# Optimization experiments

Measured on AMD Instinct MI355X. Metric: run time of the kernel, lower is better.

Reference implementation:

```python
import jax, jax.numpy as jnp
import numpy as np


def _chamfer(x, y):
    """pytorch3d.loss.chamfer_distance with defaults:
    mean over points in each direction, sum of the two directions, mean over batch.
    x: [B, N, 3], y: [B, M, 3]; squared Euclidean distances.
    """
    d = (jnp.sum(x * x, axis=-1)[:, :, None]
         + jnp.sum(y * y, axis=-1)[:, None, :]
         - 2.0 * jnp.einsum('bnd,bmd->bnm', x, y))
    cham_x = jnp.mean(jnp.min(d, axis=2), axis=1)  # [B] mean over N of NN dist in y
    cham_y = jnp.mean(jnp.min(d, axis=1), axis=1)  # [B] mean over M of NN dist in x
    return jnp.mean(cham_x) + jnp.mean(cham_y)


def setup_inputs() -> dict:
    key = jax.random.key(0)
    k1, k2, k3 = jax.random.split(key, 3)
    B, N_COARSE, N_FINE, N_GT = 8, 1024, 8192, 8192
    coarse = jax.random.normal(k1, (B, N_COARSE, 3), dtype=jnp.float32)
    fine = jax.random.normal(k2, (B, N_FINE, 3), dtype=jnp.float32)
    gt = jax.random.normal(k3, (B, 3, N_GT), dtype=jnp.float32)  # channel-first, transposed in forward
    alpha = jnp.ones((), dtype=jnp.float32)
    return {"coarse": coarse, "fine": fine, "gt": gt, "alpha": alpha}


def reference(coarse, fine, gt, alpha):
    gt_pts = jnp.transpose(gt, (0, 2, 1))  # [B, N_gt, 3]
    loss_fine = _chamfer(fine, gt_pts)
    loss_coarse = _chamfer(coarse, gt_pts)
    loss = loss_coarse + alpha * loss_fine
    return (loss, loss_coarse, loss_fine)
```

## Files before the change

kernel.cpp:

```cpp
#include <hip/hip_runtime.h>
#include <math.h>

#define TPB 256
#define NF 8192
#define NC 1024
#define NG 8192
#define GRID 4608

#define NMIN 204800
#define RED_BLOCKS 200

typedef _Float16 h8 __attribute__((ext_vector_type(8)));
typedef float fx16 __attribute__((ext_vector_type(16)));

__device__ __forceinline__ float min3f(float a, float b, float c) {
    return fminf(fminf(a, b), c);
}

__global__ __launch_bounds__(TPB) void chamfer_mfma(
    const float* __restrict__ coarse, const float* __restrict__ fine,
    const float* __restrict__ gt, unsigned int* __restrict__ wsmin,
    float* __restrict__ ctrl)
{
    __shared__ __align__(16) _Float16 sA[4096];

    const int bid = blockIdx.x;
    const int tid = threadIdx.x;

    if (bid == 0 && tid < 4) ((unsigned int*)ctrl)[tid] = 0u;

    const float* qp; const float* tp;
    int Nq, Nt; bool qcf, tcf; int batch, qblk, t0, tcount, qbase;

    if (bid < 2048) {
        qp = fine; tp = gt; Nq = NF; Nt = NG; qcf = false; tcf = true;
        batch = bid >> 8; qblk = (bid >> 3) & 31; t0 = (bid & 7) * 1024; tcount = 1024;
        qbase = 0 + batch * NF;
    } else if (bid < 4096) {
        const int r = bid - 2048;
        qp = gt; tp = fine; Nq = NG; Nt = NF; qcf = true; tcf = false;
        batch = r >> 8; qblk = (r >> 3) & 31; t0 = (r & 7) * 1024; tcount = 1024;
        qbase = 65536 + batch * NG;
    } else if (bid < 4352) {
        const int r = bid - 4096;
        qp = coarse; tp = gt; Nq = NC; Nt = NG; qcf = false; tcf = true;
        batch = r >> 5; qblk = (r >> 3) & 3; t0 = (r & 7) * 1024; tcount = 1024;
        qbase = 196608 + batch * NC;
    } else {
        const int r = bid - 4352;
        qp = gt; tp = coarse; Nq = NG; Nt = NC; qcf = true; tcf = false;
        batch = r >> 5; qblk = r & 31; t0 = 0; tcount = 1024;
        qbase = 131072 + batch * NG;
    }

    const int lane = tid & 63;
    const int wave = tid >> 6;
    const int qrow = lane & 31;
    const int kg   = lane >> 5;

    const _Float16 n2  = (_Float16)(-2.0f);
    const _Float16 one = (_Float16)(1.0f);
    const _Float16 zro = (_Float16)(0.0f);

    h8 bq[2]; float qs2[2]; float mmin[2];
#pragma unroll
    for (int j = 0; j < 2; j++) {
        const int qi = qblk * 256 + wave * 64 + j * 32 + qrow;
        float x, y, z;
        if (qcf) {
            x = qp[(size_t)(batch * 3 + 0) * Nq + qi];
            y = qp[(size_t)(batch * 3 + 1) * Nq + qi];
            z = qp[(size_t)(batch * 3 + 2) * Nq + qi];
        } else {
            const float* p = qp + ((size_t)batch * Nq + qi) * 3;
            x = p[0]; y = p[1]; z = p[2];
        }
        qs2[j] = x * x + y * y + z * z;
        const _Float16 xh = (_Float16)x, yh = (_Float16)y, zh = (_Float16)z;
        const _Float16 xl = (_Float16)(x - (float)xh);
        const _Float16 yl = (_Float16)(y - (float)yh);
        const _Float16 zl = (_Float16)(z - (float)zh);
        h8 f;
        if (kg == 0) {
            f[0] = n2 * xh; f[1] = n2 * yh; f[2] = n2 * zh;
            f[3] = n2 * xh; f[4] = n2 * yh; f[5] = n2 * zh;
            f[6] = n2 * xl; f[7] = n2 * yl;
        } else {
            f[0] = n2 * zl; f[1] = one; f[2] = one;
            f[3] = zro; f[4] = zro; f[5] = zro; f[6] = zro; f[7] = zro;
        }
        bq[j] = f;
        mmin[j] = INFINITY;
    }

    const fx16 zacc = {0.f,0.f,0.f,0.f,0.f,0.f,0.f,0.f,
                       0.f,0.f,0.f,0.f,0.f,0.f,0.f,0.f};

    for (int base = 0; base < tcount; base += 256) {
        const int tj = t0 + base + tid;
        float x, y, z;
        if (tcf) {
            x = tp[(size_t)(batch * 3 + 0) * Nt + tj];
            y = tp[(size_t)(batch * 3 + 1) * Nt + tj];
            z = tp[(size_t)(batch * 3 + 2) * Nt + tj];
        } else {
            const float* p = tp + ((size_t)batch * Nt + tj) * 3;
            x = p[0]; y = p[1]; z = p[2];
        }
        const float s = x * x + y * y + z * z;
        const _Float16 xh = (_Float16)x, yh = (_Float16)y, zh = (_Float16)z;
        const _Float16 xl = (_Float16)(x - (float)xh);
        const _Float16 yl = (_Float16)(y - (float)yh);
        const _Float16 zl = (_Float16)(z - (float)zh);
        const _Float16 sh = (_Float16)s;
        const _Float16 sl = (_Float16)(s - (float)sh);
        h8 k0, k1;
        k0[0] = xh; k0[1] = yh; k0[2] = zh; k0[3] = xl;
        k0[4] = yl; k0[5] = zl; k0[6] = xh; k0[7] = yh;
        k1[0] = zh; k1[1] = sh; k1[2] = sl; k1[3] = zro;
        k1[4] = zro; k1[5] = zro; k1[6] = zro; k1[7] = zro;

        __syncthreads();
        const int tr = tid & 31, tt = tid >> 5;
        *(h8*)&sA[tt * 512 + tr * 8]       = k0;
        *(h8*)&sA[tt * 512 + 256 + tr * 8] = k1;
        __syncthreads();

#pragma unroll 4
        for (int tile = 0; tile < 8; tile++) {
            const h8 af = *(const h8*)&sA[tile * 512 + lane * 8];
            const fx16 d0 = __builtin_amdgcn_mfma_f32_32x32x16_f16(af, bq[0], zacc, 0, 0, 0);
            const fx16 d1 = __builtin_amdgcn_mfma_f32_32x32x16_f16(af, bq[1], zacc, 0, 0, 0);
            mmin[0] = min3f(min3f(min3f(d0[0], d0[1], d0[2]),
                                  min3f(d0[3], d0[4], d0[5]),
                                  min3f(d0[6], d0[7], d0[8])),
                            min3f(min3f(d0[9], d0[10], d0[11]),
                                  min3f(d0[12], d0[13], d0[14]),
                                  d0[15]),
                            mmin[0]);
            mmin[1] = min3f(min3f(min3f(d1[0], d1[1], d1[2]),
                                  min3f(d1[3], d1[4], d1[5]),
                                  min3f(d1[6], d1[7], d1[8])),
                            min3f(min3f(d1[9], d1[10], d1[11]),
                                  min3f(d1[12], d1[13], d1[14]),
                                  d1[15]),
                            mmin[1]);
        }
    }

#pragma unroll
    for (int j = 0; j < 2; j++)
        mmin[j] = fminf(mmin[j], __shfl_xor(mmin[j], 32));

    const int qi = qblk * 256 + wave * 64 + kg * 32 + qrow;
    const float d = mmin[kg] + qs2[kg];
    atomicMin(&wsmin[qbase + qi], __float_as_uint(d));
}

__global__ __launch_bounds__(256) void reduce_final_kernel(
    const uint4* __restrict__ wsmin4,
    float* __restrict__ ctrl,
    const float* __restrict__ alpha,
    float* __restrict__ out)
{
    __shared__ float red0[4], red1[4];
    const int tid = threadIdx.x;
    const int i = blockIdx.x * 256 + tid;

    const uint4 v = wsmin4[i];
    const float sum4 = __uint_as_float(v.x) + __uint_as_float(v.y)
                     + __uint_as_float(v.z) + __uint_as_float(v.w);
    float s0 = 0.0f, s1 = 0.0f;
    if (i < 32768)      s0 = sum4 * (1.0f / 65536.0f);
    else if (i < 49152) s1 = sum4 * (1.0f / 65536.0f);
    else                s1 = sum4 * (1.0f / 8192.0f);

    for (int off = 32; off > 0; off >>= 1) {
        s0 += __shfl_down(s0, off);
        s1 += __shfl_down(s1, off);
    }
    if ((tid & 63) == 0) { red0[tid >> 6] = s0; red1[tid >> 6] = s1; }
    __syncthreads();
    if (tid == 0) {
        atomicAdd(&ctrl[0], red0[0] + red0[1] + red0[2] + red0[3]);
        atomicAdd(&ctrl[1], red1[0] + red1[1] + red1[2] + red1[3]);
        __threadfence();
        const unsigned old = atomicAdd((unsigned int*)&ctrl[2], 1u);
        if (old == RED_BLOCKS - 1) {
            const float lf = atomicAdd(&ctrl[0], 0.0f);
            const float lc = atomicAdd(&ctrl[1], 0.0f);
            out[0] = lc + alpha[0] * lf;
            out[1] = lc;
            out[2] = lf;
        }
    }
}

extern "C" void kernel_launch(void* const* d_in, const int* in_sizes, int n_in,
                              void* d_out, int out_size, void* d_ws, size_t ws_size,
                              hipStream_t stream) {
    const float* coarse = (const float*)d_in[0];
    const float* fine   = (const float*)d_in[1];
    const float* gt     = (const float*)d_in[2];
    const float* alpha  = (const float*)d_in[3];
    float* out = (float*)d_out;
    unsigned int* wsmin = (unsigned int*)d_ws;
    float* ctrl = (float*)((char*)d_ws + (size_t)NMIN * 4);

    chamfer_mfma<<<GRID, TPB, 0, stream>>>(coarse, fine, gt, wsmin, ctrl);
    reduce_final_kernel<<<RED_BLOCKS, 256, 0, stream>>>((const uint4*)wsmin, ctrl, alpha, out);
}
```

Baseline: 120.7 us.

## Widen per-wave query tile to four MFMA blocks and prefetch next target chunk

Each wave now holds four 32-query B fragments instead of two, so each shared-memory A fragment feeds four MFMAs. Target chunks grow to 512 points, and each block covers a 2048-target span. The next chunk's coordinates are loaded into registers while the current chunk is being processed. The grid shrinks from 4608 to 1216 blocks, which reduces redundant target staging, global loads and atomicMin traffic. The cost is higher register pressure, double the LDS use and fewer blocks to balance across CUs.

```diff
diff --git a/kernel.cpp b/kernel.cpp
--- a/kernel.cpp
+++ b/kernel.cpp
@@ -5,7 +5,8 @@
 #define NF 8192
 #define NC 1024
 #define NG 8192
-#define GRID 4608
+#define GRID 1216
+#define CHUNK 512
 
 #define NMIN 204800
 #define RED_BLOCKS 200
@@ -15,6 +16,16 @@
 
 __device__ __forceinline__ float min3f(float a, float b, float c) {
     return fminf(fminf(a, b), c);
+}
+
+__device__ __forceinline__ float red16(const fx16 d, float carry) {
+    return min3f(min3f(min3f(d[0], d[1], d[2]),
+                       min3f(d[3], d[4], d[5]),
+                       min3f(d[6], d[7], d[8])),
+                 min3f(min3f(d[9], d[10], d[11]),
+                       min3f(d[12], d[13], d[14]),
+                       d[15]),
+                 carry);
 }
 
 __global__ __launch_bounds__(TPB) void chamfer_mfma(
@@ -22,7 +33,7 @@
     const float* __restrict__ gt, unsigned int* __restrict__ wsmin,
     float* __restrict__ ctrl)
 {
-    __shared__ __align__(16) _Float16 sA[4096];
+    __shared__ __align__(16) _Float16 sA[8192];
 
     const int bid = blockIdx.x;
     const int tid = threadIdx.x;
@@ -32,24 +43,24 @@
     const float* qp; const float* tp;
     int Nq, Nt; bool qcf, tcf; int batch, qblk, t0, tcount, qbase;
 
-    if (bid < 2048) {
+    if (bid < 512) {
         qp = fine; tp = gt; Nq = NF; Nt = NG; qcf = false; tcf = true;
-        batch = bid >> 8; qblk = (bid >> 3) & 31; t0 = (bid & 7) * 1024; tcount = 1024;
+        batch = bid >> 6; qblk = (bid >> 2) & 15; t0 = (bid & 3) * 2048; tcount = 2048;
         qbase = 0 + batch * NF;
-    } else if (bid < 4096) {
-        const int r = bid - 2048;
+    } else if (bid < 1024) {
+        const int r = bid - 512;
         qp = gt; tp = fine; Nq = NG; Nt = NF; qcf = true; tcf = false;
-        batch = r >> 8; qblk = (r >> 3) & 31; t0 = (r & 7) * 1024; tcount = 1024;
+        batch = r >> 6; qblk = (r >> 2) & 15; t0 = (r & 3) * 2048; tcount = 2048;
         qbase = 65536 + batch * NG;
-    } else if (bid < 4352) {
-        const int r = bid - 4096;
+    } else if (bid < 1088) {
+        const int r = bid - 1024;
         qp = coarse; tp = gt; Nq = NC; Nt = NG; qcf = false; tcf = true;
-        batch = r >> 5; qblk = (r >> 3) & 3; t0 = (r & 7) * 1024; tcount = 1024;
+        batch = r >> 3; qblk = (r >> 2) & 1; t0 = (r & 3) * 2048; tcount = 2048;
         qbase = 196608 + batch * NC;
     } else {
-        const int r = bid - 4352;
+        const int r = bid - 1088;
         qp = gt; tp = coarse; Nq = NG; Nt = NC; qcf = true; tcf = false;
-        batch = r >> 5; qblk = r & 31; t0 = 0; tcount = 1024;
+        batch = r >> 4; qblk = r & 15; t0 = 0; tcount = 1024;
         qbase = 131072 + batch * NG;
     }
 
@@ -62,10 +73,10 @@
     const _Float16 one = (_Float16)(1.0f);
     const _Float16 zro = (_Float16)(0.0f);
 
-    h8 bq[2]; float qs2[2]; float mmin[2];
-#pragma unroll
-    for (int j = 0; j < 2; j++) {
-        const int qi = qblk * 256 + wave * 64 + j * 32 + qrow;
+    h8 bq[4]; float qs2[4]; float mmin[4];
+#pragma unroll
+    for (int j = 0; j < 4; j++) {
+        const int qi = qblk * 512 + wave * 128 + j * 32 + qrow;
         float x, y, z;
         if (qcf) {
             x = qp[(size_t)(batch * 3 + 0) * Nq + qi];
@@ -96,65 +107,86 @@
     const fx16 zacc = {0.f,0.f,0.f,0.f,0.f,0.f,0.f,0.f,
                        0.f,0.f,0.f,0.f,0.f,0.f,0.f,0.f};
 
-    for (int base = 0; base < tcount; base += 256) {
-        const int tj = t0 + base + tid;
-        float x, y, z;
+    float px[2], py[2], pz[2];
+#pragma unroll
+    for (int u = 0; u < 2; u++) {
+        const int tj = t0 + u * 256 + tid;
         if (tcf) {
-            x = tp[(size_t)(batch * 3 + 0) * Nt + tj];
-            y = tp[(size_t)(batch * 3 + 1) * Nt + tj];
-            z = tp[(size_t)(batch * 3 + 2) * Nt + tj];
+            px[u] = tp[(size_t)(batch * 3 + 0) * Nt + tj];
+            py[u] = tp[(size_t)(batch * 3 + 1) * Nt + tj];
+            pz[u] = tp[(size_t)(batch * 3 + 2) * Nt + tj];
         } else {
             const float* p = tp + ((size_t)batch * Nt + tj) * 3;
-            x = p[0]; y = p[1]; z = p[2];
-        }
-        const float s = x * x + y * y + z * z;
-        const _Float16 xh = (_Float16)x, yh = (_Float16)y, zh = (_Float16)z;
-        const _Float16 xl = (_Float16)(x - (float)xh);
-        const _Float16 yl = (_Float16)(y - (float)yh);
-        const _Float16 zl = (_Float16)(z - (float)zh);
-        const _Float16 sh = (_Float16)s;
-        const _Float16 sl = (_Float16)(s - (float)sh);
-        h8 k0, k1;
-        k0[0] = xh; k0[1] = yh; k0[2] = zh; k0[3] = xl;
-        k0[4] = yl; k0[5] = zl; k0[6] = xh; k0[7] = yh;
-        k1[0] = zh; k1[1] = sh; k1[2] = sl; k1[3] = zro;
-        k1[4] = zro; k1[5] = zro; k1[6] = zro; k1[7] = zro;
-
+            px[u] = p[0]; py[u] = p[1]; pz[u] = p[2];
+        }
+    }
+
+    const int nchunks = tcount >> 9;
+    for (int c = 0; c < nchunks; c++) {
         __syncthreads();
-        const int tr = tid & 31, tt = tid >> 5;
-        *(h8*)&sA[tt * 512 + tr * 8]       = k0;
-        *(h8*)&sA[tt * 512 + 256 + tr * 8] = k1;
+#pragma unroll
+        for (int u = 0; u < 2; u++) {
+            const float x = px[u], y = py[u], z = pz[u];
+            const float s = x * x + y * y + z * z;
+            const _Float16 xh = (_Float16)x, yh = (_Float16)y, zh = (_Float16)z;
+            const _Float16 xl = (_Float16)(x - (float)xh);
+            const _Float16 yl = (_Float16)(y - (float)yh);
+            const _Float16 zl = (_Float16)(z - (float)zh);
+            const _Float16 sh = (_Float16)s;
+            const _Float16 sl = (_Float16)(s - (float)sh);
+            h8 k0, k1;
+            k0[0] = xh; k0[1] = yh; k0[2] = zh; k0[3] = xl;
+            k0[4] = yl; k0[5] = zl; k0[6] = xh; k0[7] = yh;
+            k1[0] = zh; k1[1] = sh; k1[2] = sl; k1[3] = zro;
+            k1[4] = zro; k1[5] = zro; k1[6] = zro; k1[7] = zro;
+            const int idx = u * 256 + tid;
+            const int tt = idx >> 5, tr = idx & 31;
+            *(h8*)&sA[tt * 512 + tr * 8]       = k0;
+            *(h8*)&sA[tt * 512 + 256 + tr * 8] = k1;
+        }
         __syncthreads();
 
+        if (c + 1 < nchunks) {
+            const int tb = t0 + (c + 1) * CHUNK;
+#pragma unroll
+            for (int u = 0; u < 2; u++) {
+                const int tj = tb + u * 256 + tid;
+                if (tcf) {
+                    px[u] = tp[(size_t)(batch * 3 + 0) * Nt + tj];
+                    py[u] = tp[(size_t)(batch * 3 + 1) * Nt + tj];
+                    pz[u] = tp[(size_t)(batch * 3 + 2) * Nt + tj];
+                } else {
+                    const float* p = tp + ((size_t)batch * Nt + tj) * 3;
+                    px[u] = p[0]; py[u] = p[1]; pz[u] = p[2];
+                }
+            }
+        }
+
 #pragma unroll 4
-        for (int tile = 0; tile < 8; tile++) {
+        for (int tile = 0; tile < 16; tile++) {
             const h8 af = *(const h8*)&sA[tile * 512 + lane * 8];
             const fx16 d0 = __builtin_amdgcn_mfma_f32_32x32x16_f16(af, bq[0], zacc, 0, 0, 0);
             const fx16 d1 = __builtin_amdgcn_mfma_f32_32x32x16_f16(af, bq[1], zacc, 0, 0, 0);
-            mmin[0] = min3f(min3f(min3f(d0[0], d0[1], d0[2]),
-                                  min3f(d0[3], d0[4], d0[5]),
-                                  min3f(d0[6], d0[7], d0[8])),
-                            min3f(min3f(d0[9], d0[10], d0[11]),
-                                  min3f(d0[12], d0[13], d0[14]),
-                                  d0[15]),
-                            mmin[0]);
-            mmin[1] = min3f(min3f(min3f(d1[0], d1[1], d1[2]),
-                                  min3f(d1[3], d1[4], d1[5]),
-                                  min3f(d1[6], d1[7], d1[8])),
-                            min3f(min3f(d1[9], d1[10], d1[11]),
-                                  min3f(d1[12], d1[13], d1[14]),
-                                  d1[15]),
-                            mmin[1]);
-        }
-    }
-
-#pragma unroll
-    for (int j = 0; j < 2; j++)
+            const fx16 d2 = __builtin_amdgcn_mfma_f32_32x32x16_f16(af, bq[2], zacc, 0, 0, 0);
+            const fx16 d3 = __builtin_amdgcn_mfma_f32_32x32x16_f16(af, bq[3], zacc, 0, 0, 0);
+            mmin[0] = red16(d0, mmin[0]);
+            mmin[1] = red16(d1, mmin[1]);
+            mmin[2] = red16(d2, mmin[2]);
+            mmin[3] = red16(d3, mmin[3]);
+        }
+    }
+
+#pragma unroll
+    for (int j = 0; j < 4; j++)
         mmin[j] = fminf(mmin[j], __shfl_xor(mmin[j], 32));
 
-    const int qi = qblk * 256 + wave * 64 + kg * 32 + qrow;
-    const float d = mmin[kg] + qs2[kg];
-    atomicMin(&wsmin[qbase + qi], __float_as_uint(d));
+    const float ma = kg ? mmin[2] : mmin[0];
+    const float mb = kg ? mmin[3] : mmin[1];
+    const float sa = kg ? qs2[2] : qs2[0];
+    const float sb = kg ? qs2[3] : qs2[1];
+    const int qa = qblk * 512 + wave * 128 + kg * 64 + qrow;
+    atomicMin(&wsmin[qbase + qa],      __float_as_uint(ma + sa));
+    atomicMin(&wsmin[qbase + qa + 32], __float_as_uint(mb + sb));
 }
 
 __global__ __launch_bounds__(256) void reduce_final_kernel(
```

New measurement: 124.5 us. +3.1%, slower.
